# Kernel tuning notes

Measured on AMD Instinct MI355X. Metric: run time of the kernel, lower is better.

The kernel has to match this reference:

```python
import jax, jax.numpy as jnp
import numpy as np

N_NODES = 65536
N_GRAPHS = 1024
NODES_PER_G = 64
N_EDGES = 1048576
IN_FEATS = 512
HIDDEN = 1024
H4 = 256
EMB = 512
EPS = 1e-5
SLOPE = 0.01


def setup_inputs() -> dict:
    key = jax.random.key(0)
    ks = jax.random.split(key, 10)
    # within-graph random edges: edge e belongs to graph e // (E/B)
    epg = N_EDGES // N_GRAPHS
    eg = np.arange(N_EDGES) // epg
    rng = np.random.default_rng(0)
    src = rng.integers(0, NODES_PER_G, N_EDGES) + eg * NODES_PER_G
    dst = rng.integers(0, NODES_PER_G, N_EDGES) + eg * NODES_PER_G
    node_gid = np.arange(N_NODES) // NODES_PER_G
    return {
        "node_feats": jax.random.normal(ks[0], (N_NODES, IN_FEATS), jnp.float32),
        "edge_weights": jax.random.uniform(ks[1], (N_EDGES,), jnp.float32),
        "W1": jax.random.normal(ks[2], (IN_FEATS, HIDDEN), jnp.float32) * 0.05,
        "W2": jax.random.normal(ks[3], (HIDDEN, H4), jnp.float32) * 0.05,
        "W_emb": jax.random.normal(ks[4], (IN_FEATS + HIDDEN + H4, EMB), jnp.float32) * 0.02,
        "gn1_alpha": jnp.ones((HIDDEN,), jnp.float32),
        "gn1_gamma": jnp.ones((HIDDEN,), jnp.float32),
        "gn1_beta": jnp.zeros((HIDDEN,), jnp.float32),
        "gn2_alpha": jnp.ones((H4,), jnp.float32),
        "gn2_gamma": jnp.ones((H4,), jnp.float32),
        "gn2_beta": jnp.zeros((H4,), jnp.float32),
        "edge_src": jnp.asarray(src, jnp.int32),
        "edge_dst": jnp.asarray(dst, jnp.int32),
        "node_gid": jnp.asarray(node_gid, jnp.int32),
    }


def _seg_sum(x, ids, num):
    return jax.ops.segment_sum(x, ids, num_segments=num)


def _graph_conv(x, W, src, dst, ew):
    # DGL GraphConv, norm='both', bias=False, with edge_weight (u_mul_e)
    ones = jnp.ones((src.shape[0],), x.dtype)
    deg_out = jnp.clip(_seg_sum(ones, src, N_NODES), 1.0)
    deg_in = jnp.clip(_seg_sum(ones, dst, N_NODES), 1.0)
    h = (x * jax.lax.rsqrt(deg_out)[:, None]) @ W
    msg = h[src] * ew[:, None]
    agg = _seg_sum(msg, dst, N_NODES)
    return agg * jax.lax.rsqrt(deg_in)[:, None]


def _graph_norm(x, gid, counts, alpha, gamma, beta):
    # GraphNorm (Cai et al.): learnable mean-scale alpha, per-graph stats
    mean = _seg_sum(x, gid, N_GRAPHS) / counts[:, None]
    sub = x - alpha * mean[gid]
    var = _seg_sum(sub * sub, gid, N_GRAPHS) / counts[:, None]
    return gamma * sub * jax.lax.rsqrt(var[gid] + EPS) + beta


def _mean_nodes(x, gid, counts):
    return _seg_sum(x, gid, N_GRAPHS) / counts[:, None]


def _leaky(x):
    return jnp.where(x >= 0, x, SLOPE * x)


def reference(node_feats, edge_weights, W1, W2, W_emb,
              gn1_alpha, gn1_gamma, gn1_beta,
              gn2_alpha, gn2_gamma, gn2_beta,
              edge_src, edge_dst, node_gid):
    counts = jnp.clip(_seg_sum(jnp.ones((N_NODES,), node_feats.dtype), node_gid, N_GRAPHS), 1.0)
    r0 = _mean_nodes(node_feats, node_gid, counts)                 # [B, in]
    h1 = _graph_conv(node_feats, W1, edge_src, edge_dst, edge_weights)
    h1 = _leaky(_graph_norm(h1, node_gid, counts, gn1_alpha, gn1_gamma, gn1_beta))
    r1 = _mean_nodes(h1, node_gid, counts)                          # [B, hidden]
    h2 = _graph_conv(h1, W2, edge_src, edge_dst, edge_weights)
    h2 = _leaky(_graph_norm(h2, node_gid, counts, gn2_alpha, gn2_gamma, gn2_beta))
    r2 = _mean_nodes(h2, node_gid, counts)                          # [B, hidden/4]
    emb = jnp.concatenate([r0, r1, r2], axis=1) @ W_emb             # [B, EMB]
    # InstanceNorm1d on [B, E] input: per-row normalization, no affine
    mu = jnp.mean(emb, axis=1, keepdims=True)
    var = jnp.mean((emb - mu) ** 2, axis=1, keepdims=True)
    emb = (emb - mu) * jax.lax.rsqrt(var + EPS)
    return _leaky(emb)
```

## Files before the change

kernel.cpp:

```cpp
#include <hip/hip_runtime.h>
#include <hip/hip_bf16.h>
#include <stdint.h>

#define N_NODES   65536
#define N_GRAPHS  1024
#define N_EDGES   1048576
#define IN_FEATS  512
#define HIDDEN    1024
#define H4        256
#define EMB_DIM   512
#define RDIM      1792
#define EPS_F     1e-5f
#define SLOPE_F   0.01f

typedef __bf16 bf16;
typedef __bf16 bf16x8 __attribute__((ext_vector_type(8)));
typedef float  floatx4 __attribute__((ext_vector_type(4)));

#define GLDS16(gp, lp) __builtin_amdgcn_global_load_lds( \
    (const __attribute__((address_space(1))) void*)(gp), \
    (__attribute__((address_space(3))) void*)(lp), 16, 0, 0)

#define MFMA16(a, b, c) __builtin_amdgcn_mfma_f32_16x16x32_bf16((a), (b), (c), 0, 0, 0)

__global__ __launch_bounds__(256) void k_graph_build(
    const int* __restrict__ src, const int* __restrict__ dst,
    const float* __restrict__ ew,
    bf16* __restrict__ adjb, float* __restrict__ scl_o)
{
    __shared__ float sAdj[4096];
    __shared__ float sDegO[64], sDegI[64];
    int g = blockIdx.x, tid = threadIdx.x;
    for (int i = tid; i < 4096; i += 256) sAdj[i] = 0.f;
    if (tid < 64) { sDegO[tid] = 0.f; sDegI[tid] = 0.f; }
    __syncthreads();
    int e0 = g * 1024;
    #pragma unroll
    for (int i = 0; i < 4; ++i) {
        int e = e0 + i * 256 + tid;
        int s = src[e] & 63, d = dst[e] & 63;
        atomicAdd(&sAdj[(d << 6) | s], ew[e]);
        atomicAdd(&sDegO[s], 1.f);
        atomicAdd(&sDegI[d], 1.f);
    }
    __syncthreads();
    if (tid < 64) scl_o[g * 64 + tid] = rsqrtf(fmaxf(sDegO[tid], 1.f));
    bf16* ag = adjb + ((size_t)g << 12);
    for (int i = tid; i < 4096; i += 256) {
        float si = rsqrtf(fmaxf(sDegI[i >> 6], 1.f));
        ag[i] = (bf16)(sAdj[i] * si);
    }
}

__global__ __launch_bounds__(256) void k_transpose_all(
    const float* __restrict__ W1, const float* __restrict__ W2,
    const float* __restrict__ Wemb,
    bf16* __restrict__ W1T, bf16* __restrict__ W2T, bf16* __restrict__ WembT)
{
    int idx = blockIdx.x * 256 + threadIdx.x;
    if (idx < 524288) {
        int n = idx & 1023, k = idx >> 10;
        W1T[(size_t)n * 512 + k] = (bf16)W1[idx];
    } else if (idx < 786432) {
        int i = idx - 524288;
        int n = i & 255, k = i >> 8;
        W2T[(size_t)n * 1024 + k] = (bf16)W2[i];
    } else {
        int i = idx - 786432;
        int n = i & 511, k = i >> 9;
        WembT[(size_t)n * 1792 + k] = (bf16)Wemb[i];
    }
}

__global__ __launch_bounds__(256) void k_prep_agg1(
    const float* __restrict__ x, const float* __restrict__ so,
    const bf16* __restrict__ adjb,
    bf16* __restrict__ axs1, bf16* __restrict__ Rb)
{
    __shared__ __align__(16) bf16 sOut[64 * 264];
    __shared__ float sSo[64];
    int g = blockIdx.x >> 1, half = blockIdx.x & 1;
    int tid = threadIdx.x, lane = tid & 63, wave = tid >> 6, q = lane >> 4;
    if (tid < 64) sSo[tid] = so[g * 64 + tid];
    const float* xg = x + (size_t)g * 64 * IN_FEATS + half * 256;
    const bf16* ag = adjb + ((size_t)g << 12);

    bf16x8 af[4][2];
    #pragma unroll
    for (int mt = 0; mt < 4; ++mt)
        #pragma unroll
        for (int kk = 0; kk < 2; ++kk)
            af[mt][kk] = *(const bf16x8*)&ag[(mt * 16 + (lane & 15)) * 64 + kk * 32 + q * 8];
    __syncthreads();
    float sov[2][8];
    #pragma unroll
    for (int kk = 0; kk < 2; ++kk)
        #pragma unroll
        for (int j = 0; j < 8; ++j) sov[kk][j] = sSo[kk * 32 + q * 8 + j];

    #pragma unroll
    for (int nt = 0; nt < 4; ++nt) {
        int cl = wave * 64 + nt * 16 + (lane & 15);
        floatx4 acc[4] = {};
        float r0 = 0.f;
        #pragma unroll
        for (int kk = 0; kk < 2; ++kk) {
            bf16x8 bfrag;
            #pragma unroll
            for (int j = 0; j < 8; ++j) {
                float v = xg[(size_t)(kk * 32 + q * 8 + j) * IN_FEATS + cl];
                r0 += v;
                bfrag[j] = (bf16)(v * sov[kk][j]);
            }
            #pragma unroll
            for (int mt = 0; mt < 4; ++mt)
                acc[mt] = MFMA16(af[mt][kk], bfrag, acc[mt]);
        }
        r0 += __shfl_xor(r0, 16);
        r0 += __shfl_xor(r0, 32);
        if (lane < 16) Rb[(size_t)g * RDIM + half * 256 + cl] = (bf16)(r0 * (1.f / 64.f));
        #pragma unroll
        for (int mt = 0; mt < 4; ++mt)
            #pragma unroll
            for (int i = 0; i < 4; ++i)
                sOut[(mt * 16 + q * 4 + i) * 264 + cl] = (bf16)acc[mt][i];
    }
    __syncthreads();
    #pragma unroll
    for (int it = 0; it < 8; ++it) {
        int idx = it * 256 + tid;
        int d = idx >> 5, c8 = idx & 31;
        *(bf16x8*)&axs1[(size_t)(g * 64 + d) * IN_FEATS + half * 256 + c8 * 8] =
            *(const bf16x8*)&sOut[d * 264 + c8 * 8];
    }
}

__device__ __forceinline__ void gemm_mainloop(
    const bf16* __restrict__ A, const bf16* __restrict__ BT, int K,
    int row0, int col0, int lane, int wave, int wm, int wn, int q,
    bf16* sA, bf16* sB, floatx4 (&acc)[4][4])
{
    for (int k0 = 0; k0 < K; k0 += 64) {
        #pragma unroll
        for (int i = 0; i < 4; ++i) {
            int u = (wave * 4 + i) * 64 + lane;
            int r = u >> 3, p = u & 7;
            int c = p ^ (r & 7);
            GLDS16(A  + (size_t)(row0 + r) * K + (k0 + c * 8), &sA[(wave * 4 + i) * 512]);
            GLDS16(BT + (size_t)(col0 + r) * K + (k0 + c * 8), &sB[(wave * 4 + i) * 512]);
        }
        asm volatile("s_waitcnt vmcnt(0)" ::: "memory");
        __syncthreads();
        #pragma unroll
        for (int kk = 0; kk < 64; kk += 32) {
            bf16x8 afr[4], bfr[4];
            #pragma unroll
            for (int mt = 0; mt < 4; ++mt) {
                int r = wm * 64 + mt * 16 + (lane & 15);
                int c = (kk >> 3) + q;
                afr[mt] = *(const bf16x8*)&sA[(r * 8 + (c ^ (r & 7))) * 8];
            }
            #pragma unroll
            for (int nt = 0; nt < 4; ++nt) {
                int r = wn * 64 + nt * 16 + (lane & 15);
                int c = (kk >> 3) + q;
                bfr[nt] = *(const bf16x8*)&sB[(r * 8 + (c ^ (r & 7))) * 8];
            }
            #pragma unroll
            for (int mt = 0; mt < 4; ++mt)
                #pragma unroll
                for (int nt = 0; nt < 4; ++nt)
                    acc[mt][nt] = MFMA16(afr[mt], bfr[nt], acc[mt][nt]);
        }
        __syncthreads();
    }
}

__device__ __forceinline__ void swizzle_block(int cb, int& bx, int& by)
{
    int b = blockIdx.y * gridDim.x + blockIdx.x;
    int xcd = b & 7, t = b >> 3;
    bx = t % cb;
    by = (t / cb) * 8 + xcd;
}

__global__ __launch_bounds__(256) void k_gemm1_f(
    const bf16* __restrict__ A, const bf16* __restrict__ BT,
    const float* __restrict__ alpha, const float* __restrict__ gamma,
    const float* __restrict__ beta,
    const float* __restrict__ so,
    bf16* __restrict__ xs2, bf16* __restrict__ Rb)
{
    __shared__ __align__(16) bf16 sm[128 * 136];
    __shared__ float sSo[128];
    bf16* sA = sm;
    bf16* sB = sm + 8192;
    const int tid = threadIdx.x;
    const int lane = tid & 63, wave = tid >> 6, q = lane >> 4;
    const int wm = wave & 1, wn = wave >> 1;
    int bx, by; swizzle_block(gridDim.x, bx, by);
    const int row0 = by * 128, col0 = bx * 128;

    if (tid < 128) sSo[tid] = so[row0 + tid];

    floatx4 acc[4][4] = {};
    gemm_mainloop(A, BT, IN_FEATS, row0, col0, lane, wave, wm, wn, q, sA, sB, acc);

    const int gw = by * 2 + wm;
    bf16* sOut = sm;
    #pragma unroll
    for (int nt = 0; nt < 4; ++nt) {
        int cl = wn * 64 + nt * 16 + (lane & 15);
        int colg = col0 + cl;
        float lsum = 0.f;
        #pragma unroll
        for (int mt = 0; mt < 4; ++mt)
            #pragma unroll
            for (int i = 0; i < 4; ++i) lsum += acc[mt][nt][i];
        lsum += __shfl_xor(lsum, 16);
        lsum += __shfl_xor(lsum, 32);
        float am = alpha[colg] * (lsum * (1.f / 64.f));
        float gm = gamma[colg], bt = beta[colg];
        float sub[4][4], qv = 0.f;
        #pragma unroll
        for (int mt = 0; mt < 4; ++mt)
            #pragma unroll
            for (int i = 0; i < 4; ++i) {
                float d = acc[mt][nt][i] - am;
                sub[mt][i] = d; qv += d * d;
            }
        qv += __shfl_xor(qv, 16);
        qv += __shfl_xor(qv, 32);
        float rs = rsqrtf(qv * (1.f / 64.f) + EPS_F);
        float rsum = 0.f;
        #pragma unroll
        for (int mt = 0; mt < 4; ++mt)
            #pragma unroll
            for (int i = 0; i < 4; ++i) {
                float o = gm * sub[mt][i] * rs + bt;
                o = (o >= 0.f) ? o : SLOPE_F * o;
                rsum += o;
                int r = wm * 64 + mt * 16 + q * 4 + i;
                sOut[r * 136 + cl] = (bf16)(o * sSo[r]);
            }
        rsum += __shfl_xor(rsum, 16);
        rsum += __shfl_xor(rsum, 32);
        if (lane < 16)
            Rb[(size_t)gw * RDIM + 512 + colg] = (bf16)(rsum * (1.f / 64.f));
    }
    __syncthreads();
    #pragma unroll
    for (int it = 0; it < 8; ++it) {
        int idx = it * 256 + tid;
        int r = idx >> 4, c8 = idx & 15;
        *(bf16x8*)&xs2[(size_t)(row0 + r) * HIDDEN + col0 + c8 * 8] =
            *(const bf16x8*)&sOut[r * 136 + c8 * 8];
    }
}

__global__ __launch_bounds__(256) void k_gemm2_f(
    const bf16* __restrict__ A, const bf16* __restrict__ BT,
    const bf16* __restrict__ adjb,
    const float* __restrict__ alpha, const float* __restrict__ gamma,
    const float* __restrict__ beta,
    bf16* __restrict__ Rb)
{
    __shared__ __align__(16) bf16 sm[20480];
    bf16* sA = sm;
    bf16* sB = sm + 4096;
    const int g = blockIdx.x, tid = threadIdx.x;
    const int lane = tid & 63, wave = tid >> 6, q = lane >> 4, l15 = lane & 15;

    floatx4 acc[4][4] = {};
    const bf16* Ag = A + ((size_t)g << 6) * HIDDEN;

    for (int k0 = 0; k0 < HIDDEN; k0 += 64) {
        {
            #pragma unroll
            for (int i = 0; i < 2; ++i) {
                int u = i * 256 + tid;
                int r = u >> 3, c = (u & 7) ^ (r & 7);
                GLDS16(Ag + (size_t)r * HIDDEN + (k0 + c * 8), &sA[(i * 256 + wave * 64) * 8]);
            }
            #pragma unroll
            for (int i = 0; i < 8; ++i) {
                int u = i * 256 + tid;
                int r = u >> 3, c = (u & 7) ^ (r & 7);
                GLDS16(BT + (size_t)r * HIDDEN + (k0 + c * 8), &sB[(i * 256 + wave * 64) * 8]);
            }
        }
        asm volatile("s_waitcnt vmcnt(0)" ::: "memory");
        __syncthreads();
        #pragma unroll
        for (int kk = 0; kk < 64; kk += 32) {
            bf16x8 afr[4], bfr[4];
            #pragma unroll
            for (int mt = 0; mt < 4; ++mt) {
                int r = mt * 16 + l15;
                int c = (kk >> 3) + q;
                afr[mt] = *(const bf16x8*)&sA[(r * 8 + (c ^ (r & 7))) * 8];
            }
            #pragma unroll
            for (int nt = 0; nt < 4; ++nt) {
                int r = wave * 64 + nt * 16 + l15;
                int c = (kk >> 3) + q;
                bfr[nt] = *(const bf16x8*)&sB[(r * 8 + (c ^ (r & 7))) * 8];
            }
            #pragma unroll
            for (int mt = 0; mt < 4; ++mt)
                #pragma unroll
                for (int nt = 0; nt < 4; ++nt)
                    acc[mt][nt] = MFMA16(afr[mt], bfr[nt], acc[mt][nt]);
        }
        __syncthreads();
    }

    bf16* sT = sm + wave * (64 * 68);
    #pragma unroll
    for (int nt = 0; nt < 4; ++nt) {
        int cl = nt * 16 + l15;
        #pragma unroll
        for (int mt = 0; mt < 4; ++mt)
            #pragma unroll
            for (int i = 0; i < 4; ++i)
                sT[cl * 68 + mt * 16 + q * 4 + i] = (bf16)acc[mt][nt][i];
    }
    asm volatile("s_waitcnt lgkmcnt(0)" ::: "memory");

    const bf16* ag = adjb + ((size_t)g << 12);
    floatx4 a2[4][4] = {};
    #pragma unroll
    for (int kk = 0; kk < 2; ++kk) {
        bf16x8 afr[4], bfr[4];
        #pragma unroll
        for (int mt = 0; mt < 4; ++mt)
            afr[mt] = *(const bf16x8*)&ag[(mt * 16 + l15) * 64 + kk * 32 + q * 8];
        #pragma unroll
        for (int nt = 0; nt < 4; ++nt)
            bfr[nt] = *(const bf16x8*)&sT[(nt * 16 + l15) * 68 + kk * 32 + q * 8];
        #pragma unroll
        for (int mt = 0; mt < 4; ++mt)
            #pragma unroll
            for (int nt = 0; nt < 4; ++nt)
                a2[mt][nt] = MFMA16(afr[mt], bfr[nt], a2[mt][nt]);
    }

    #pragma unroll
    for (int nt = 0; nt < 4; ++nt) {
        int colg = wave * 64 + nt * 16 + l15;
        float lsum = 0.f;
        #pragma unroll
        for (int mt = 0; mt < 4; ++mt)
            #pragma unroll
            for (int i = 0; i < 4; ++i) lsum += a2[mt][nt][i];
        lsum += __shfl_xor(lsum, 16);
        lsum += __shfl_xor(lsum, 32);
        float am = alpha[colg] * (lsum * (1.f / 64.f));
        float gm = gamma[colg], bt = beta[colg];
        float sub[4][4], qv = 0.f;
        #pragma unroll
        for (int mt = 0; mt < 4; ++mt)
            #pragma unroll
            for (int i = 0; i < 4; ++i) {
                float d = a2[mt][nt][i] - am;
                sub[mt][i] = d; qv += d * d;
            }
        qv += __shfl_xor(qv, 16);
        qv += __shfl_xor(qv, 32);
        float rs = rsqrtf(qv * (1.f / 64.f) + EPS_F);
        float rsum = 0.f;
        #pragma unroll
        for (int mt = 0; mt < 4; ++mt)
            #pragma unroll
            for (int i = 0; i < 4; ++i) {
                float o = gm * sub[mt][i] * rs + bt;
                rsum += (o >= 0.f) ? o : SLOPE_F * o;
            }
        rsum += __shfl_xor(rsum, 16);
        rsum += __shfl_xor(rsum, 32);
        if (lane < 16)
            Rb[(size_t)g * RDIM + 1536 + colg] = (bf16)(rsum * (1.f / 64.f));
    }
}

__global__ __launch_bounds__(256) void k_gemm_ro(
    const bf16* __restrict__ A, const bf16* __restrict__ BT,
    float* __restrict__ Cout)
{
    __shared__ __align__(16) bf16 sm[16384];
    bf16* sA = sm;
    bf16* sB = sm + 8192;
    const int tid = threadIdx.x;
    const int lane = tid & 63, wave = tid >> 6, q = lane >> 4;
    const int wm = wave & 1, wn = wave >> 1;
    const int row0 = blockIdx.y * 128, col0 = blockIdx.x * 128;

    floatx4 acc[4][4] = {};
    gemm_mainloop(A, BT, RDIM, row0, col0, lane, wave, wm, wn, q, sA, sB, acc);

    #pragma unroll
    for (int mt = 0; mt < 4; ++mt)
        #pragma unroll
        for (int nt = 0; nt < 4; ++nt) {
            int col = col0 + wn * 64 + nt * 16 + (lane & 15);
            #pragma unroll
            for (int i = 0; i < 4; ++i) {
                int row = row0 + wm * 64 + mt * 16 + q * 4 + i;
                Cout[(size_t)row * EMB_DIM + col] = acc[mt][nt][i];
            }
        }
}

__global__ __launch_bounds__(256) void k_instnorm(
    const float* __restrict__ emb, float* __restrict__ out)
{
    int row = blockIdx.x, tid = threadIdx.x;
    int lane = tid & 63, wave = tid >> 6;
    __shared__ float sS[4], sQ[4];
    float v0 = emb[(size_t)row * EMB_DIM + tid];
    float v1 = emb[(size_t)row * EMB_DIM + 256 + tid];
    float s = v0 + v1, q = v0 * v0 + v1 * v1;
    #pragma unroll
    for (int off = 32; off; off >>= 1) {
        s += __shfl_down(s, off);
        q += __shfl_down(q, off);
    }
    if (lane == 0) { sS[wave] = s; sQ[wave] = q; }
    __syncthreads();
    float S = sS[0] + sS[1] + sS[2] + sS[3];
    float Q = sQ[0] + sQ[1] + sQ[2] + sQ[3];
    float mu = S * (1.f / 512.f);
    float var = Q * (1.f / 512.f) - mu * mu;
    float rs = rsqrtf(var + EPS_F);
    float o0 = (v0 - mu) * rs; o0 = (o0 >= 0.f) ? o0 : SLOPE_F * o0;
    float o1 = (v1 - mu) * rs; o1 = (o1 >= 0.f) ? o1 : SLOPE_F * o1;
    out[(size_t)row * EMB_DIM + tid]       = o0;
    out[(size_t)row * EMB_DIM + 256 + tid] = o1;
}

extern "C" void kernel_launch(void* const* d_in, const int* in_sizes, int n_in,
                              void* d_out, int out_size, void* d_ws, size_t ws_size,
                              hipStream_t stream) {
    const float* x    = (const float*)d_in[0];
    const float* ew   = (const float*)d_in[1];
    const float* W1   = (const float*)d_in[2];
    const float* W2   = (const float*)d_in[3];
    const float* Wemb = (const float*)d_in[4];
    const float* a1   = (const float*)d_in[5];
    const float* g1   = (const float*)d_in[6];
    const float* b1   = (const float*)d_in[7];
    const float* a2   = (const float*)d_in[8];
    const float* g2   = (const float*)d_in[9];
    const float* b2   = (const float*)d_in[10];
    const int* esrc   = (const int*)d_in[11];
    const int* edst   = (const int*)d_in[12];
    float* out = (float*)d_out;

    char* ws = (char*)d_ws;
    const size_t MB = 1024ull * 1024ull;
    bf16*  adjb   = (bf16*)(ws);
    float* scl_o  = (float*)(ws + 8 * MB);
    bf16*  Rb     = (bf16*)(ws + 9 * MB);
    bf16*  W1T    = (bf16*)(ws + 13 * MB);
    bf16*  W2T    = (bf16*)(ws + 14 * MB);
    bf16*  WembT  = (bf16*)(ws + 15 * MB);
    float* emb    = (float*)(ws + 17 * MB);
    bf16*  axs1   = (bf16*)(ws + 20 * MB);
    bf16*  xs2    = (bf16*)(ws + 84 * MB);

    k_graph_build<<<N_GRAPHS, 256, 0, stream>>>(esrc, edst, ew, adjb, scl_o);
    k_transpose_all<<<6656, 256, 0, stream>>>(W1, W2, Wemb, W1T, W2T, WembT);

    k_prep_agg1<<<N_GRAPHS * 2, 256, 0, stream>>>(x, scl_o, adjb, axs1, Rb);

    k_gemm1_f<<<dim3(HIDDEN / 128, N_NODES / 128), 256, 0, stream>>>(
        axs1, W1T, a1, g1, b1, scl_o, xs2, Rb);
    k_gemm2_f<<<N_GRAPHS, 256, 0, stream>>>(
        xs2, W2T, adjb, a2, g2, b2, Rb);
    k_gemm_ro<<<dim3(EMB_DIM / 128, N_GRAPHS / 128), 256, 0, stream>>>(
        Rb, WembT, emb);
    k_instnorm<<<N_GRAPHS, 256, 0, stream>>>(emb, out);

    (void)in_sizes; (void)n_in; (void)out_size; (void)ws_size;
}
```

Baseline: 491.7 us.

## Double-buffer A tiles, load B directly to registers, split-K readout GEMM, tiled transpose

Replaces the shared GEMM mainloop with a double-buffered loop that stages only A in LDS and reads B fragments straight from global memory into registers, which overlaps the next A load with the current MFMAs. The readout GEMM is split four ways along K into partial buffers that the instance-norm kernel sums, giving that small GEMM more blocks. The weight transpose now goes through a 32x32 shared-memory tile so both reads and writes are coalesced. The direct B loads depend on cache hits and could raise global traffic, and the split-K adds extra partial-sum traffic.

```diff
diff --git a/kernel.cpp b/kernel.cpp
--- a/kernel.cpp
+++ b/kernel.cpp
@@ -52,24 +52,25 @@
     }
 }
 
-__global__ __launch_bounds__(256) void k_transpose_all(
+__global__ __launch_bounds__(256) void k_transpose_tiled(
     const float* __restrict__ W1, const float* __restrict__ W2,
     const float* __restrict__ Wemb,
     bf16* __restrict__ W1T, bf16* __restrict__ W2T, bf16* __restrict__ WembT)
 {
-    int idx = blockIdx.x * 256 + threadIdx.x;
-    if (idx < 524288) {
-        int n = idx & 1023, k = idx >> 10;
-        W1T[(size_t)n * 512 + k] = (bf16)W1[idx];
-    } else if (idx < 786432) {
-        int i = idx - 524288;
-        int n = i & 255, k = i >> 8;
-        W2T[(size_t)n * 1024 + k] = (bf16)W2[i];
-    } else {
-        int i = idx - 786432;
-        int n = i & 511, k = i >> 9;
-        WembT[(size_t)n * 1792 + k] = (bf16)Wemb[i];
-    }
+    int b = blockIdx.x, tid = threadIdx.x;
+    const float* W; bf16* WT; int K, N, kt, nt;
+    if (b < 512)      { W = W1;   WT = W1T;   K = 512;  N = 1024; kt = b >> 5;  nt = b & 31; }
+    else if (b < 768) { int i = b - 512; W = W2;   WT = W2T;   K = 1024; N = 256;  kt = i >> 3;  nt = i & 7; }
+    else              { int i = b - 768; W = Wemb; WT = WembT; K = 1792; N = 512;  kt = i >> 4;  nt = i & 15; }
+    __shared__ float t[32][33];
+    int c = tid & 31, r8 = tid >> 5;
+    #pragma unroll
+    for (int rr = 0; rr < 32; rr += 8)
+        t[rr + r8][c] = W[(size_t)(kt * 32 + rr + r8) * N + nt * 32 + c];
+    __syncthreads();
+    #pragma unroll
+    for (int rr = 0; rr < 32; rr += 8)
+        WT[(size_t)(nt * 32 + rr + r8) * K + kt * 32 + c] = (bf16)t[c][rr + r8];
 }
 
 __global__ __launch_bounds__(256) void k_prep_agg1(
@@ -135,44 +136,62 @@
     }
 }
 
-__device__ __forceinline__ void gemm_mainloop(
-    const bf16* __restrict__ A, const bf16* __restrict__ BT, int K,
-    int row0, int col0, int lane, int wave, int wm, int wn, int q,
-    bf16* sA, bf16* sB, floatx4 (&acc)[4][4])
-{
-    for (int k0 = 0; k0 < K; k0 += 64) {
-        #pragma unroll
-        for (int i = 0; i < 4; ++i) {
-            int u = (wave * 4 + i) * 64 + lane;
-            int r = u >> 3, p = u & 7;
-            int c = p ^ (r & 7);
-            GLDS16(A  + (size_t)(row0 + r) * K + (k0 + c * 8), &sA[(wave * 4 + i) * 512]);
-            GLDS16(BT + (size_t)(col0 + r) * K + (k0 + c * 8), &sB[(wave * 4 + i) * 512]);
-        }
+template<int ROWS>
+__device__ __forceinline__ void kloop_bdirect(
+    const bf16* __restrict__ Abase,
+    const bf16* __restrict__ bp,
+    int K, int k0_start, int niter,
+    bf16* __restrict__ sbuf0, bf16* __restrict__ sbuf1,
+    int rbase, int tid, int wave, int q, int l15,
+    floatx4 (&acc)[4][4])
+{
+    constexpr int UPT = ROWS * 8 / 256;
+    #pragma unroll
+    for (int i = 0; i < UPT; ++i) {
+        int u = i * 256 + tid;
+        int r = u >> 3, c = (u & 7) ^ (r & 7);
+        GLDS16(Abase + (size_t)r * K + (k0_start + c * 8), &sbuf0[(i * 256 + wave * 64) * 8]);
+    }
+    for (int it = 0; it < niter; ++it) {
+        int k0 = k0_start + it * 64;
+        bf16* cur = (it & 1) ? sbuf1 : sbuf0;
+        bf16* nxt = (it & 1) ? sbuf0 : sbuf1;
         asm volatile("s_waitcnt vmcnt(0)" ::: "memory");
         __syncthreads();
-        #pragma unroll
-        for (int kk = 0; kk < 64; kk += 32) {
-            bf16x8 afr[4], bfr[4];
-            #pragma unroll
-            for (int mt = 0; mt < 4; ++mt) {
-                int r = wm * 64 + mt * 16 + (lane & 15);
-                int c = (kk >> 3) + q;
-                afr[mt] = *(const bf16x8*)&sA[(r * 8 + (c ^ (r & 7))) * 8];
-            }
-            #pragma unroll
-            for (int nt = 0; nt < 4; ++nt) {
-                int r = wn * 64 + nt * 16 + (lane & 15);
-                int c = (kk >> 3) + q;
-                bfr[nt] = *(const bf16x8*)&sB[(r * 8 + (c ^ (r & 7))) * 8];
-            }
-            #pragma unroll
-            for (int mt = 0; mt < 4; ++mt)
-                #pragma unroll
-                for (int nt = 0; nt < 4; ++nt)
-                    acc[mt][nt] = MFMA16(afr[mt], bfr[nt], acc[mt][nt]);
+        if (it + 1 < niter) {
+            #pragma unroll
+            for (int i = 0; i < UPT; ++i) {
+                int u = i * 256 + tid;
+                int r = u >> 3, c = (u & 7) ^ (r & 7);
+                GLDS16(Abase + (size_t)r * K + (k0 + 64 + c * 8), &nxt[(i * 256 + wave * 64) * 8]);
+            }
         }
-        __syncthreads();
+        const bf16* bpk = bp + k0;
+        bf16x8 b0[4], b1[4], afr[4];
+        #pragma unroll
+        for (int nt = 0; nt < 4; ++nt) b0[nt] = *(const bf16x8*)(bpk + (size_t)nt * 16 * K);
+        #pragma unroll
+        for (int nt = 0; nt < 4; ++nt) b1[nt] = *(const bf16x8*)(bpk + (size_t)nt * 16 * K + 32);
+        #pragma unroll
+        for (int mt = 0; mt < 4; ++mt) {
+            int r = rbase + mt * 16 + l15;
+            afr[mt] = *(const bf16x8*)&cur[(r * 8 + (q ^ (r & 7))) * 8];
+        }
+        #pragma unroll
+        for (int mt = 0; mt < 4; ++mt)
+            #pragma unroll
+            for (int nt = 0; nt < 4; ++nt)
+                acc[mt][nt] = MFMA16(afr[mt], b0[nt], acc[mt][nt]);
+        #pragma unroll
+        for (int mt = 0; mt < 4; ++mt) {
+            int r = rbase + mt * 16 + l15;
+            afr[mt] = *(const bf16x8*)&cur[(r * 8 + ((4 + q) ^ (r & 7))) * 8];
+        }
+        #pragma unroll
+        for (int mt = 0; mt < 4; ++mt)
+            #pragma unroll
+            for (int nt = 0; nt < 4; ++nt)
+                acc[mt][nt] = MFMA16(afr[mt], b1[nt], acc[mt][nt]);
     }
 }
 
@@ -193,10 +212,8 @@
 {
     __shared__ __align__(16) bf16 sm[128 * 136];
     __shared__ float sSo[128];
-    bf16* sA = sm;
-    bf16* sB = sm + 8192;
     const int tid = threadIdx.x;
-    const int lane = tid & 63, wave = tid >> 6, q = lane >> 4;
+    const int lane = tid & 63, wave = tid >> 6, q = lane >> 4, l15 = lane & 15;
     const int wm = wave & 1, wn = wave >> 1;
     int bx, by; swizzle_block(gridDim.x, bx, by);
     const int row0 = by * 128, col0 = bx * 128;
@@ -204,13 +221,17 @@
     if (tid < 128) sSo[tid] = so[row0 + tid];
 
     floatx4 acc[4][4] = {};
-    gemm_mainloop(A, BT, IN_FEATS, row0, col0, lane, wave, wm, wn, q, sA, sB, acc);
+    kloop_bdirect<128>(A + (size_t)row0 * IN_FEATS,
+                       BT + (size_t)(col0 + wn * 64 + l15) * IN_FEATS + q * 8,
+                       IN_FEATS, 0, 8, sm, sm + 8192,
+                       wm * 64, tid, wave, q, l15, acc);
+    __syncthreads();
 
     const int gw = by * 2 + wm;
     bf16* sOut = sm;
     #pragma unroll
     for (int nt = 0; nt < 4; ++nt) {
-        int cl = wn * 64 + nt * 16 + (lane & 15);
+        int cl = wn * 64 + nt * 16 + l15;
         int colg = col0 + cl;
         float lsum = 0.f;
         #pragma unroll
@@ -265,55 +286,16 @@
     const float* __restrict__ beta,
     bf16* __restrict__ Rb)
 {
-    __shared__ __align__(16) bf16 sm[20480];
-    bf16* sA = sm;
-    bf16* sB = sm + 4096;
+    __shared__ __align__(16) bf16 sm[128 * 136];
     const int g = blockIdx.x, tid = threadIdx.x;
     const int lane = tid & 63, wave = tid >> 6, q = lane >> 4, l15 = lane & 15;
 
     floatx4 acc[4][4] = {};
-    const bf16* Ag = A + ((size_t)g << 6) * HIDDEN;
-
-    for (int k0 = 0; k0 < HIDDEN; k0 += 64) {
-        {
-            #pragma unroll
-            for (int i = 0; i < 2; ++i) {
-                int u = i * 256 + tid;
-                int r = u >> 3, c = (u & 7) ^ (r & 7);
-                GLDS16(Ag + (size_t)r * HIDDEN + (k0 + c * 8), &sA[(i * 256 + wave * 64) * 8]);
-            }
-            #pragma unroll
-            for (int i = 0; i < 8; ++i) {
-                int u = i * 256 + tid;
-                int r = u >> 3, c = (u & 7) ^ (r & 7);
-                GLDS16(BT + (size_t)r * HIDDEN + (k0 + c * 8), &sB[(i * 256 + wave * 64) * 8]);
-            }
-        }
-        asm volatile("s_waitcnt vmcnt(0)" ::: "memory");
-        __syncthreads();
-        #pragma unroll
-        for (int kk = 0; kk < 64; kk += 32) {
-            bf16x8 afr[4], bfr[4];
-            #pragma unroll
-            for (int mt = 0; mt < 4; ++mt) {
-                int r = mt * 16 + l15;
-                int c = (kk >> 3) + q;
-                afr[mt] = *(const bf16x8*)&sA[(r * 8 + (c ^ (r & 7))) * 8];
-            }
-            #pragma unroll
-            for (int nt = 0; nt < 4; ++nt) {
-                int r = wave * 64 + nt * 16 + l15;
-                int c = (kk >> 3) + q;
-                bfr[nt] = *(const bf16x8*)&sB[(r * 8 + (c ^ (r & 7))) * 8];
-            }
-            #pragma unroll
-            for (int mt = 0; mt < 4; ++mt)
-                #pragma unroll
-                for (int nt = 0; nt < 4; ++nt)
-                    acc[mt][nt] = MFMA16(afr[mt], bfr[nt], acc[mt][nt]);
-        }
-        __syncthreads();
-    }
+    kloop_bdirect<64>(A + ((size_t)g << 6) * HIDDEN,
+                      BT + (size_t)(wave * 64 + l15) * HIDDEN + q * 8,
+                      HIDDEN, 0, 16, sm, sm + 4096,
+                      0, tid, wave, q, l15, acc);
+    __syncthreads();
 
     bf16* sT = sm + wave * (64 * 68);
     #pragma unroll
@@ -385,24 +367,27 @@
 
 __global__ __launch_bounds__(256) void k_gemm_ro(
     const bf16* __restrict__ A, const bf16* __restrict__ BT,
-    float* __restrict__ Cout)
+    float* __restrict__ embP)
 {
     __shared__ __align__(16) bf16 sm[16384];
-    bf16* sA = sm;
-    bf16* sB = sm + 8192;
     const int tid = threadIdx.x;
-    const int lane = tid & 63, wave = tid >> 6, q = lane >> 4;
+    const int lane = tid & 63, wave = tid >> 6, q = lane >> 4, l15 = lane & 15;
     const int wm = wave & 1, wn = wave >> 1;
     const int row0 = blockIdx.y * 128, col0 = blockIdx.x * 128;
+    const int kz = blockIdx.z;
 
     floatx4 acc[4][4] = {};
-    gemm_mainloop(A, BT, RDIM, row0, col0, lane, wave, wm, wn, q, sA, sB, acc);
-
+    kloop_bdirect<128>(A + (size_t)row0 * RDIM,
+                       BT + (size_t)(col0 + wn * 64 + l15) * RDIM + q * 8,
+                       RDIM, kz * 448, 7, sm, sm + 8192,
+                       wm * 64, tid, wave, q, l15, acc);
+
+    float* Cout = embP + (size_t)kz * (N_GRAPHS * EMB_DIM);
     #pragma unroll
     for (int mt = 0; mt < 4; ++mt)
         #pragma unroll
         for (int nt = 0; nt < 4; ++nt) {
-            int col = col0 + wn * 64 + nt * 16 + (lane & 15);
+            int col = col0 + wn * 64 + nt * 16 + l15;
             #pragma unroll
             for (int i = 0; i < 4; ++i) {
                 int row = row0 + wm * 64 + mt * 16 + q * 4 + i;
@@ -412,13 +397,15 @@
 }
 
 __global__ __launch_bounds__(256) void k_instnorm(
-    const float* __restrict__ emb, float* __restrict__ out)
-{
+    const float* __restrict__ embP, float* __restrict__ out)
+{
+    const int P = N_GRAPHS * EMB_DIM;
     int row = blockIdx.x, tid = threadIdx.x;
     int lane = tid & 63, wave = tid >> 6;
     __shared__ float sS[4], sQ[4];
-    float v0 = emb[(size_t)row * EMB_DIM + tid];
-    float v1 = emb[(size_t)row * EMB_DIM + 256 + tid];
+    size_t b = (size_t)row * EMB_DIM + tid;
+    float v0 = embP[b] + embP[b + P] + embP[b + 2 * P] + embP[b + 3 * P];
+    float v1 = embP[b + 256] + embP[b + 256 + P] + embP[b + 256 + 2 * P] + embP[b + 256 + 3 * P];
     float s = v0 + v1, q = v0 * v0 + v1 * v1;
     #pragma unroll
     for (int off = 32; off; off >>= 1) {
@@ -464,12 +451,12 @@
     bf16*  W1T    = (bf16*)(ws + 13 * MB);
     bf16*  W2T    = (bf16*)(ws + 14 * MB);
     bf16*  WembT  = (bf16*)(ws + 15 * MB);
-    float* emb    = (float*)(ws + 17 * MB);
-    bf16*  axs1   = (bf16*)(ws + 20 * MB);
-    bf16*  xs2    = (bf16*)(ws + 84 * MB);
+    float* embP   = (float*)(ws + 17 * MB);
+    bf16*  axs1   = (bf16*)(ws + 25 * MB);
+    bf16*  xs2    = (bf16*)(ws + 89 * MB);
 
     k_graph_build<<<N_GRAPHS, 256, 0, stream>>>(esrc, edst, ew, adjb, scl_o);
-    k_transpose_all<<<6656, 256, 0, stream>>>(W1, W2, Wemb, W1T, W2T, WembT);
+    k_transpose_tiled<<<1664, 256, 0, stream>>>(W1, W2, Wemb, W1T, W2T, WembT);
 
     k_prep_agg1<<<N_GRAPHS * 2, 256, 0, stream>>>(x, scl_o, adjb, axs1, Rb);
 
@@ -477,9 +464,9 @@
         axs1, W1T, a1, g1, b1, scl_o, xs2, Rb);
     k_gemm2_f<<<N_GRAPHS, 256, 0, stream>>>(
         xs2, W2T, adjb, a2, g2, b2, Rb);
-    k_gemm_ro<<<dim3(EMB_DIM / 128, N_GRAPHS / 128), 256, 0, stream>>>(
-        Rb, WembT, emb);
-    k_instnorm<<<N_GRAPHS, 256, 0, stream>>>(emb, out);
+    k_gemm_ro<<<dim3(EMB_DIM / 128, N_GRAPHS / 128, 4), 256, 0, stream>>>(
+        Rb, WembT, embP);
+    k_instnorm<<<N_GRAPHS, 256, 0, stream>>>(embP, out);
 
     (void)in_sizes; (void)n_in; (void)out_size; (void)ws_size;
 }
```

Measured after the change: 524.1 us. 6.6% more time.
